# Performance work log

Measured on AMD Instinct MI355X. Metric: run time of the kernel, lower is better.

The kernel has to match this reference:

```python
import jax, jax.numpy as jnp
import numpy as np

B, T, I, H, O = 64, 512, 128, 1024, 128
FORGET_BIAS = 1.0  # TF LSTMCell default


def setup_inputs() -> dict:
    key = jax.random.key(0)
    k1, k2, k3 = jax.random.split(key, 3)
    X = jax.random.normal(k1, (B, T, I), dtype=jnp.float32)
    Wk = jax.random.normal(k2, (I + H, 4 * H), dtype=jnp.float32) * 0.02
    b = jnp.zeros((4 * H,), dtype=jnp.float32)
    Wd = jax.random.normal(k3, (H, O), dtype=jnp.float32) * 0.02
    bd = jnp.zeros((O,), dtype=jnp.float32)
    return {"X": X, "Wk": Wk, "b": b, "Wd": Wd, "bd": bd}


def _lstm(X, Wk, b):
    # TF LSTMCell with activation=relu; gate order in kernel: i, j, f, o
    batch = X.shape[0]
    h = X.shape[-1]  # not used; keep shapes explicit below
    c0 = jnp.zeros((batch, H), dtype=X.dtype)
    h0 = jnp.zeros((batch, H), dtype=X.dtype)

    def step(carry, x_t):
        c, hs = carry
        z = jnp.concatenate([x_t, hs], axis=-1) @ Wk + b  # [B, 4H]
        i, j, f, o = jnp.split(z, 4, axis=-1)
        i = jax.nn.sigmoid(i)
        f = jax.nn.sigmoid(f + FORGET_BIAS)
        o = jax.nn.sigmoid(o)
        g = jax.nn.relu(j)          # cell-input activation (custom relu)
        c_new = f * c + i * g
        h_new = o * jax.nn.relu(c_new)  # output activation (custom relu)
        return (c_new, h_new), h_new

    xs = jnp.swapaxes(X, 0, 1)  # [T, B, I]
    _, hs = jax.lax.scan(step, (c0, h0), xs)
    return jnp.swapaxes(hs, 0, 1)  # [B, T, H]


def reference(X, Wk, b, Wd, bd):
    rnn_out = _lstm(X, Wk, b)          # [B, T, H]
    outputs = rnn_out @ Wd + bd        # [B, T, O] (SL=True: dense per timestep)
    return outputs
```

## Files before the change

kernel.cpp:

```cpp
#include <hip/hip_runtime.h>
#include <math.h>

#define Bsz 64
#define Tn  512
#define In  128
#define Hn  1024
#define KT  1152
#define NBLK 128

#define GARR0 0
#define GFLG0 512

typedef __attribute__((ext_vector_type(8))) short bf16x8;
typedef __attribute__((ext_vector_type(4))) short s16x4;
typedef __attribute__((ext_vector_type(4))) float f32x4;
typedef __attribute__((ext_vector_type(4))) int   i32x4;

__device__ void llvm_amdgcn_raw_buffer_store_i16(short vdata, i32x4 srsrc, int voffset, int soffset, int cpol) __asm("llvm.amdgcn.raw.buffer.store.i16");

__device__ __forceinline__ i32x4 make_srd(const void* p, int bytes) {
  i32x4 r;
  r.x = (int)(unsigned)(unsigned long long)p;
  r.y = (int)((unsigned long long)p >> 32);
  r.z = bytes;
  r.w = 0x00020000;
  return r;
}

__device__ __forceinline__ unsigned short f2bf(float f) {
  union { float f; unsigned u; } x; x.f = f;
  unsigned r = x.u + 0x7FFFu + ((x.u >> 16) & 1u);
  return (unsigned short)(r >> 16);
}
__device__ __forceinline__ float sigmoidf_(float x) { return 1.0f / (1.0f + __expf(-x)); }

__global__ __launch_bounds__(256) void cast_x_kernel(const float* __restrict__ in,
                                                     unsigned short* __restrict__ out) {
  int i = blockIdx.x * 256 + threadIdx.x;
  f32x4 v = ((const f32x4*)in)[i];
  s16x4 o;
  o.x = (short)f2bf(v.x); o.y = (short)f2bf(v.y);
  o.z = (short)f2bf(v.z); o.w = (short)f2bf(v.w);
  ((s16x4*)out)[i] = o;
}

__global__ __launch_bounds__(256) void transpose_cast_kernel(const float* __restrict__ in,
                                                             unsigned short* __restrict__ out,
                                                             int R, int C, int ldo, int tilesR) {
  __shared__ unsigned short tile[64][73];
  int br = blockIdx.x % tilesR, bc = blockIdx.x / tilesR;
  int r0 = br << 6, c0 = bc << 6;
  for (int e = threadIdx.x; e < 4096; e += 256) {
    int r = e >> 6, c = e & 63;
    tile[r][c] = f2bf(in[(size_t)(r0 + r) * C + (c0 + c)]);
  }
  __syncthreads();
  for (int e = threadIdx.x; e < 4096; e += 256) {
    int c = e >> 6, r = e & 63;
    out[(size_t)(c0 + c) * ldo + (r0 + r)] = tile[r][c];
  }
}

__global__ __launch_bounds__(512, 1) void lstm_kernel(
    const unsigned short* __restrict__ Xb,
    const unsigned short* __restrict__ WkT,
    const float* __restrict__ bias,
    unsigned short* __restrict__ hs,
    unsigned* __restrict__ S)
{
  __shared__ float Z4[4][64][36];
  const int tid = threadIdx.x;
  const int blk = blockIdx.x;
  const int grp = blk >> 4;
  const int w   = tid >> 6;
  const int mh  = w & 1;
  const int kq  = w >> 1;
  const int l   = tid & 63, q = l >> 4, n16 = l & 15;

  const i32x4 hsrd = make_srd(hs, Tn * Bsz * Hn * 2);

  bf16x8 Bf[2][9];
#pragma unroll
  for (int nt = 0; nt < 2; ++nt) {
    int cl   = nt * 16 + n16;
    int gcol = (cl >> 3) * Hn + blk * 8 + (cl & 7);
    const unsigned short* bp = WkT + (size_t)gcol * KT + kq * 288 + q * 8;
#pragma unroll
    for (int ks = 0; ks < 9; ++ks)
      Bf[nt][ks] = *(const bf16x8*)(bp + ks * 32);
  }

  const int eb = tid >> 3, ej = tid & 7;
  const float bi  = bias[           blk * 8 + ej];
  const float bg  = bias[    Hn   + blk * 8 + ej];
  const float bfg = bias[2 * Hn   + blk * 8 + ej] + 1.0f;
  const float bo  = bias[3 * Hn   + blk * 8 + ej];
  const int   hst_off = (eb * Hn + blk * 8 + ej) * 2;
  float cst = 0.0f;

  const int b0 = mh * 32 + n16;
  const int b1 = b0 + 16;

  const unsigned needm = (kq == 0) ? 0x03u : (kq == 1) ? 0x0Eu : (kq == 2) ? 0x38u : 0xE0u;
  const bool mine = (l < 8) && ((needm >> l) & 1u);

  for (int t = 0; t < Tn; ++t) {
    f32x4 a00 = {0,0,0,0}, a01 = {0,0,0,0}, a10 = {0,0,0,0}, a11 = {0,0,0,0};

    if (t > 0) {
      bf16x8 X0[4], X1[4];
      if (kq == 0) {
#pragma unroll
        for (int ks = 0; ks < 4; ++ks) {
          X0[ks] = *(const bf16x8*)(Xb + ((size_t)b0 * Tn + t) * In + ks * 32 + q * 8);
          X1[ks] = *(const bf16x8*)(Xb + ((size_t)b1 * Tn + t) * In + ks * 32 + q * 8);
        }
      }
      for (;;) {
        unsigned f = mine ? __hip_atomic_load(&S[GFLG0 + 32 * l], __ATOMIC_RELAXED,
                                              __HIP_MEMORY_SCOPE_AGENT)
                          : 0xFFFFFFFFu;
        if (__ballot(f >= (unsigned)t) == ~0ull) break;
        __builtin_amdgcn_s_sleep(1);
      }
      const unsigned short* hrow = hs + (size_t)(t - 1) * (Bsz * Hn);
#pragma unroll
      for (int ks = 0; ks < 9; ++ks) {
        bf16x8 A0, A1;
        if (kq == 0 && ks < 4) {
          A0 = X0[ks]; A1 = X1[ks];
        } else {
          int kh = kq * 288 + ks * 32 - 128 + q * 8;
          A0 = *(const bf16x8*)(hrow + (size_t)b0 * Hn + kh);
          A1 = *(const bf16x8*)(hrow + (size_t)b1 * Hn + kh);
        }
        a00 = __builtin_amdgcn_mfma_f32_16x16x32_bf16(A0, Bf[0][ks], a00, 0, 0, 0);
        a01 = __builtin_amdgcn_mfma_f32_16x16x32_bf16(A0, Bf[1][ks], a01, 0, 0, 0);
        a10 = __builtin_amdgcn_mfma_f32_16x16x32_bf16(A1, Bf[0][ks], a10, 0, 0, 0);
        a11 = __builtin_amdgcn_mfma_f32_16x16x32_bf16(A1, Bf[1][ks], a11, 0, 0, 0);
      }
    } else if (kq == 0) {
#pragma unroll
      for (int ks = 0; ks < 4; ++ks) {
        bf16x8 A0 = *(const bf16x8*)(Xb + ((size_t)b0 * Tn) * In + ks * 32 + q * 8);
        bf16x8 A1 = *(const bf16x8*)(Xb + ((size_t)b1 * Tn) * In + ks * 32 + q * 8);
        a00 = __builtin_amdgcn_mfma_f32_16x16x32_bf16(A0, Bf[0][ks], a00, 0, 0, 0);
        a01 = __builtin_amdgcn_mfma_f32_16x16x32_bf16(A0, Bf[1][ks], a01, 0, 0, 0);
        a10 = __builtin_amdgcn_mfma_f32_16x16x32_bf16(A1, Bf[0][ks], a10, 0, 0, 0);
        a11 = __builtin_amdgcn_mfma_f32_16x16x32_bf16(A1, Bf[1][ks], a11, 0, 0, 0);
      }
    }

#pragma unroll
    for (int r = 0; r < 4; ++r) {
      int row = mh * 32 + q * 4 + r;
      Z4[kq][row     ][     n16] = a00[r];
      Z4[kq][row     ][16 + n16] = a01[r];
      Z4[kq][row + 16][     n16] = a10[r];
      Z4[kq][row + 16][16 + n16] = a11[r];
    }
    __syncthreads();

    float zi = bi, zg = bg, zf = bfg, zo = bo;
#pragma unroll
    for (int k2 = 0; k2 < 4; ++k2) {
      zi += Z4[k2][eb][     ej];
      zg += Z4[k2][eb][ 8 + ej];
      zf += Z4[k2][eb][16 + ej];
      zo += Z4[k2][eb][24 + ej];
    }
    float ig = sigmoidf_(zi);
    float g  = fmaxf(zg, 0.0f);
    float ff = sigmoidf_(zf);
    float oo = sigmoidf_(zo);
    cst = ff * cst + ig * g;
    float hn = oo * fmaxf(cst, 0.0f);
    llvm_amdgcn_raw_buffer_store_i16((short)f2bf(hn), hsrd,
                                     t * (Bsz * Hn * 2) + hst_off, 0, 17);

    __syncthreads();
    if (t < Tn - 1 && tid == 0) {
      const unsigned tgt = (unsigned)t + 1u;
      unsigned old = __hip_atomic_fetch_add(&S[GARR0 + 32 * grp], 1u,
                                            __ATOMIC_RELAXED, __HIP_MEMORY_SCOPE_AGENT);
      if (old == 16u * tgt - 1u)
        __hip_atomic_store(&S[GFLG0 + 32 * grp], tgt,
                           __ATOMIC_RELAXED, __HIP_MEMORY_SCOPE_AGENT);
    }
  }
}

__global__ __launch_bounds__(256) void dense_kernel(
    const unsigned short* __restrict__ hs,
    const unsigned short* __restrict__ WdT,
    const float* __restrict__ bd,
    float* __restrict__ out)
{
  const int tid = threadIdx.x;
  const int w = tid >> 6, l = tid & 63, q = l >> 4, n16 = l & 15;
  const int R0 = blockIdx.x * 64 + w * 16;
  f32x4 acc[8];
#pragma unroll
  for (int i = 0; i < 8; ++i) acc[i] = (f32x4){0, 0, 0, 0};
  const unsigned short* arow = hs + (size_t)(R0 + n16) * Hn + q * 8;
#pragma unroll 4
  for (int ks = 0; ks < 32; ++ks) {
    bf16x8 A = *(const bf16x8*)(arow + ks * 32);
#pragma unroll
    for (int nt = 0; nt < 8; ++nt) {
      bf16x8 Bf = *(const bf16x8*)(WdT + (size_t)(nt * 16 + n16) * Hn + ks * 32 + q * 8);
      acc[nt] = __builtin_amdgcn_mfma_f32_16x16x32_bf16(A, Bf, acc[nt], 0, 0, 0);
    }
  }
#pragma unroll
  for (int nt = 0; nt < 8; ++nt) {
    int col = nt * 16 + n16;
    float bdv = bd[col];
#pragma unroll
    for (int r = 0; r < 4; ++r) {
      int R = R0 + q * 4 + r;
      int b = R & 63, t = R >> 6;
      out[((size_t)b * Tn + t) * 128 + col] = acc[nt][r] + bdv;
    }
  }
}

extern "C" void kernel_launch(void* const* d_in, const int* in_sizes, int n_in,
                              void* d_out, int out_size, void* d_ws, size_t ws_size,
                              hipStream_t stream) {
  const float* X    = (const float*)d_in[0];
  const float* Wk   = (const float*)d_in[1];
  const float* bias = (const float*)d_in[2];
  const float* Wd   = (const float*)d_in[3];
  const float* bd   = (const float*)d_in[4];
  float* out = (float*)d_out;

  char* ws = (char*)d_ws;
  unsigned short* Xb  = (unsigned short*)(ws);
  unsigned short* WkT = (unsigned short*)(ws + 8388608);
  unsigned short* WdT = (unsigned short*)(ws + 17825792);
  unsigned short* hs  = (unsigned short*)(ws + 18087936);
  unsigned*       syn = (unsigned*)      (ws + 85196800);

  hipMemsetAsync(syn, 0, 4096, stream);
  cast_x_kernel<<<4096, 256, 0, stream>>>(X, Xb);
  transpose_cast_kernel<<<1152, 256, 0, stream>>>(Wk, WkT, 1152, 4096, 1152, 18);
  transpose_cast_kernel<<<32, 256, 0, stream>>>(Wd, WdT, 1024, 128, 1024, 16);
  lstm_kernel<<<NBLK, 512, 0, stream>>>(Xb, WkT, bias, hs, syn);
  dense_kernel<<<512, 256, 0, stream>>>(hs, WdT, bd, out);
}
```

Before: 3.027 ms.

## Replace atomic counter barrier with per-block flags and vectorized h stores

Drops the per-group atomic fetch_add arrival counter and flag. Each block now writes its own step flag with a plain store, issued by lane 0 after a vmcnt(0) wait. Consumers poll the flags of the blocks they depend on with 16-byte buffer loads and take the min in registers. The h output is first staged in LDS, then written with one 16-byte store per batch row instead of scattered 2-byte stores. This removes the atomic serialization and a hop from the inter-block handoff, but now relies on the wait inside one wave to order the other waves' stores ahead of the flag, which is a memory-ordering risk.

After: 4.061 ms. 34.2% more time.

```diff
diff --git a/kernel.cpp b/kernel.cpp
--- a/kernel.cpp
+++ b/kernel.cpp
@@ -8,15 +8,15 @@
 #define KT  1152
 #define NBLK 128
 
-#define GARR0 0
-#define GFLG0 512
 
 typedef __attribute__((ext_vector_type(8))) short bf16x8;
 typedef __attribute__((ext_vector_type(4))) short s16x4;
 typedef __attribute__((ext_vector_type(4))) float f32x4;
 typedef __attribute__((ext_vector_type(4))) int   i32x4;
 
-__device__ void llvm_amdgcn_raw_buffer_store_i16(short vdata, i32x4 srsrc, int voffset, int soffset, int cpol) __asm("llvm.amdgcn.raw.buffer.store.i16");
+__device__ void llvm_amdgcn_raw_buffer_store_v4i32(i32x4 vdata, i32x4 srsrc, int voffset, int soffset, int cpol) __asm("llvm.amdgcn.raw.buffer.store.v4i32");
+__device__ void llvm_amdgcn_raw_buffer_store_i32(int vdata, i32x4 srsrc, int voffset, int soffset, int cpol) __asm("llvm.amdgcn.raw.buffer.store.i32");
+__device__ i32x4 llvm_amdgcn_raw_buffer_load_v4i32(i32x4 srsrc, int voffset, int soffset, int cpol) __asm("llvm.amdgcn.raw.buffer.load.v4i32");
 
 __device__ __forceinline__ i32x4 make_srd(const void* p, int bytes) {
   i32x4 r;
@@ -69,15 +69,16 @@
     unsigned* __restrict__ S)
 {
   __shared__ float Z4[4][64][36];
+  __shared__ __align__(16) unsigned short Hl[64][8];
   const int tid = threadIdx.x;
   const int blk = blockIdx.x;
-  const int grp = blk >> 4;
   const int w   = tid >> 6;
   const int mh  = w & 1;
   const int kq  = w >> 1;
   const int l   = tid & 63, q = l >> 4, n16 = l & 15;
 
   const i32x4 hsrd = make_srd(hs, Tn * Bsz * Hn * 2);
+  const i32x4 fsrd = make_srd(S, 2048);
 
   bf16x8 Bf[2][9];
 #pragma unroll
@@ -95,14 +96,13 @@
   const float bg  = bias[    Hn   + blk * 8 + ej];
   const float bfg = bias[2 * Hn   + blk * 8 + ej] + 1.0f;
   const float bo  = bias[3 * Hn   + blk * 8 + ej];
-  const int   hst_off = (eb * Hn + blk * 8 + ej) * 2;
   float cst = 0.0f;
 
   const int b0 = mh * 32 + n16;
   const int b1 = b0 + 16;
 
-  const unsigned needm = (kq == 0) ? 0x03u : (kq == 1) ? 0x0Eu : (kq == 2) ? 0x38u : 0xE0u;
-  const bool mine = (l < 8) && ((needm >> l) & 1u);
+  const int gbase = (kq == 0) ? 0 : (5 + (kq - 1) * 9);
+  const int ng    = kq ? 9 : 5;
 
   for (int t = 0; t < Tn; ++t) {
     f32x4 a00 = {0,0,0,0}, a01 = {0,0,0,0}, a10 = {0,0,0,0}, a11 = {0,0,0,0};
@@ -117,10 +117,17 @@
         }
       }
       for (;;) {
-        unsigned f = mine ? __hip_atomic_load(&S[GFLG0 + 32 * l], __ATOMIC_RELAXED,
-                                              __HIP_MEMORY_SCOPE_AGENT)
-                          : 0xFFFFFFFFu;
-        if (__ballot(f >= (unsigned)t) == ~0ull) break;
+        asm volatile("" ::: "memory");
+        unsigned m = 0xFFFFFFFFu;
+        if (l < ng) {
+          i32x4 v = llvm_amdgcn_raw_buffer_load_v4i32(fsrd, (gbase + l) << 4, 0, 17);
+          unsigned ma = (unsigned)v.x, mb = (unsigned)v.y;
+          unsigned mc = (unsigned)v.z, md = (unsigned)v.w;
+          ma = ma < mb ? ma : mb;
+          mc = mc < md ? mc : md;
+          m  = ma < mc ? ma : mc;
+        }
+        if (__ballot(m >= (unsigned)t) == ~0ull) break;
         __builtin_amdgcn_s_sleep(1);
       }
       const unsigned short* hrow = hs + (size_t)(t - 1) * (Bsz * Hn);
@@ -175,17 +182,16 @@
     float oo = sigmoidf_(zo);
     cst = ff * cst + ig * g;
     float hn = oo * fmaxf(cst, 0.0f);
-    llvm_amdgcn_raw_buffer_store_i16((short)f2bf(hn), hsrd,
-                                     t * (Bsz * Hn * 2) + hst_off, 0, 17);
-
+    Hl[eb][ej] = f2bf(hn);
     __syncthreads();
-    if (t < Tn - 1 && tid == 0) {
-      const unsigned tgt = (unsigned)t + 1u;
-      unsigned old = __hip_atomic_fetch_add(&S[GARR0 + 32 * grp], 1u,
-                                            __ATOMIC_RELAXED, __HIP_MEMORY_SCOPE_AGENT);
-      if (old == 16u * tgt - 1u)
-        __hip_atomic_store(&S[GFLG0 + 32 * grp], tgt,
-                           __ATOMIC_RELAXED, __HIP_MEMORY_SCOPE_AGENT);
+
+    if (tid < 64) {
+      i32x4 hv = *(const i32x4*)(&Hl[tid][0]);
+      llvm_amdgcn_raw_buffer_store_v4i32(hv, hsrd,
+          t * (Bsz * Hn * 2) + (tid * Hn + blk * 8) * 2, 0, 17);
+      asm volatile("s_waitcnt vmcnt(0)" ::: "memory");
+      if (tid == 0 && t < Tn - 1)
+        llvm_amdgcn_raw_buffer_store_i32(t + 1, fsrd, blk << 2, 0, 17);
     }
   }
 }
```

## Rebalance K split across waves and poll arrival counters directly instead of flags

Applied to the files above, without the earlier changes.

Re-splits the K dimension so each of the four K-quarter waves takes 32 input columns plus 256 hidden columns. The old split gave wave 0 all 128 input columns, so its hidden slices straddled group boundaries and needed flags from up to three groups. Each wave now waits on exactly two group counters. The separate flag word, which the last arriving block had to set, is gone: waiters poll the arrival counter against 16*t, removing the second store from the critical path between timesteps. It also adds unconditional per-step X loads for every wave, and spinning now happens on a counter that is also being atomically incremented.

After: 3.602 ms. 19.0% more time.

```diff
diff --git a/kernel.cpp b/kernel.cpp
--- a/kernel.cpp
+++ b/kernel.cpp
@@ -9,7 +9,6 @@
 #define NBLK 128
 
 #define GARR0 0
-#define GFLG0 512
 
 typedef __attribute__((ext_vector_type(8))) short bf16x8;
 typedef __attribute__((ext_vector_type(4))) short s16x4;
@@ -84,10 +83,11 @@
   for (int nt = 0; nt < 2; ++nt) {
     int cl   = nt * 16 + n16;
     int gcol = (cl >> 3) * Hn + blk * 8 + (cl & 7);
-    const unsigned short* bp = WkT + (size_t)gcol * KT + kq * 288 + q * 8;
-#pragma unroll
-    for (int ks = 0; ks < 9; ++ks)
-      Bf[nt][ks] = *(const bf16x8*)(bp + ks * 32);
+    const unsigned short* bp = WkT + (size_t)gcol * KT;
+    Bf[nt][0] = *(const bf16x8*)(bp + kq * 32 + q * 8);
+#pragma unroll
+    for (int ks = 1; ks < 9; ++ks)
+      Bf[nt][ks] = *(const bf16x8*)(bp + 128 + kq * 256 + (ks - 1) * 32 + q * 8);
   }
 
   const int eb = tid >> 3, ej = tid & 7;
@@ -101,54 +101,41 @@
   const int b0 = mh * 32 + n16;
   const int b1 = b0 + 16;
 
-  const unsigned needm = (kq == 0) ? 0x03u : (kq == 1) ? 0x0Eu : (kq == 2) ? 0x38u : 0xE0u;
-  const bool mine = (l < 8) && ((needm >> l) & 1u);
-
   for (int t = 0; t < Tn; ++t) {
     f32x4 a00 = {0,0,0,0}, a01 = {0,0,0,0}, a10 = {0,0,0,0}, a11 = {0,0,0,0};
 
+    bf16x8 X0 = *(const bf16x8*)(Xb + ((size_t)b0 * Tn + t) * In + kq * 32 + q * 8);
+    bf16x8 X1 = *(const bf16x8*)(Xb + ((size_t)b1 * Tn + t) * In + kq * 32 + q * 8);
+
     if (t > 0) {
-      bf16x8 X0[4], X1[4];
-      if (kq == 0) {
-#pragma unroll
-        for (int ks = 0; ks < 4; ++ks) {
-          X0[ks] = *(const bf16x8*)(Xb + ((size_t)b0 * Tn + t) * In + ks * 32 + q * 8);
-          X1[ks] = *(const bf16x8*)(Xb + ((size_t)b1 * Tn + t) * In + ks * 32 + q * 8);
-        }
-      }
+      const unsigned tgt = 16u * (unsigned)t;
       for (;;) {
-        unsigned f = mine ? __hip_atomic_load(&S[GFLG0 + 32 * l], __ATOMIC_RELAXED,
-                                              __HIP_MEMORY_SCOPE_AGENT)
-                          : 0xFFFFFFFFu;
-        if (__ballot(f >= (unsigned)t) == ~0ull) break;
+        unsigned f = (l < 2) ? __hip_atomic_load(&S[GARR0 + 32 * (2 * kq + l)],
+                                                 __ATOMIC_RELAXED, __HIP_MEMORY_SCOPE_AGENT)
+                             : 0xFFFFFFFFu;
+        if (__ballot(f >= tgt) == ~0ull) break;
         __builtin_amdgcn_s_sleep(1);
       }
       const unsigned short* hrow = hs + (size_t)(t - 1) * (Bsz * Hn);
-#pragma unroll
-      for (int ks = 0; ks < 9; ++ks) {
-        bf16x8 A0, A1;
-        if (kq == 0 && ks < 4) {
-          A0 = X0[ks]; A1 = X1[ks];
-        } else {
-          int kh = kq * 288 + ks * 32 - 128 + q * 8;
-          A0 = *(const bf16x8*)(hrow + (size_t)b0 * Hn + kh);
-          A1 = *(const bf16x8*)(hrow + (size_t)b1 * Hn + kh);
-        }
+      a00 = __builtin_amdgcn_mfma_f32_16x16x32_bf16(X0, Bf[0][0], a00, 0, 0, 0);
+      a01 = __builtin_amdgcn_mfma_f32_16x16x32_bf16(X0, Bf[1][0], a01, 0, 0, 0);
+      a10 = __builtin_amdgcn_mfma_f32_16x16x32_bf16(X1, Bf[0][0], a10, 0, 0, 0);
+      a11 = __builtin_amdgcn_mfma_f32_16x16x32_bf16(X1, Bf[1][0], a11, 0, 0, 0);
+#pragma unroll
+      for (int ks = 1; ks < 9; ++ks) {
+        int kh = kq * 256 + (ks - 1) * 32 + q * 8;
+        bf16x8 A0 = *(const bf16x8*)(hrow + (size_t)b0 * Hn + kh);
+        bf16x8 A1 = *(const bf16x8*)(hrow + (size_t)b1 * Hn + kh);
         a00 = __builtin_amdgcn_mfma_f32_16x16x32_bf16(A0, Bf[0][ks], a00, 0, 0, 0);
         a01 = __builtin_amdgcn_mfma_f32_16x16x32_bf16(A0, Bf[1][ks], a01, 0, 0, 0);
         a10 = __builtin_amdgcn_mfma_f32_16x16x32_bf16(A1, Bf[0][ks], a10, 0, 0, 0);
         a11 = __builtin_amdgcn_mfma_f32_16x16x32_bf16(A1, Bf[1][ks], a11, 0, 0, 0);
       }
-    } else if (kq == 0) {
-#pragma unroll
-      for (int ks = 0; ks < 4; ++ks) {
-        bf16x8 A0 = *(const bf16x8*)(Xb + ((size_t)b0 * Tn) * In + ks * 32 + q * 8);
-        bf16x8 A1 = *(const bf16x8*)(Xb + ((size_t)b1 * Tn) * In + ks * 32 + q * 8);
-        a00 = __builtin_amdgcn_mfma_f32_16x16x32_bf16(A0, Bf[0][ks], a00, 0, 0, 0);
-        a01 = __builtin_amdgcn_mfma_f32_16x16x32_bf16(A0, Bf[1][ks], a01, 0, 0, 0);
-        a10 = __builtin_amdgcn_mfma_f32_16x16x32_bf16(A1, Bf[0][ks], a10, 0, 0, 0);
-        a11 = __builtin_amdgcn_mfma_f32_16x16x32_bf16(A1, Bf[1][ks], a11, 0, 0, 0);
-      }
+    } else {
+      a00 = __builtin_amdgcn_mfma_f32_16x16x32_bf16(X0, Bf[0][0], a00, 0, 0, 0);
+      a01 = __builtin_amdgcn_mfma_f32_16x16x32_bf16(X0, Bf[1][0], a01, 0, 0, 0);
+      a10 = __builtin_amdgcn_mfma_f32_16x16x32_bf16(X1, Bf[0][0], a10, 0, 0, 0);
+      a11 = __builtin_amdgcn_mfma_f32_16x16x32_bf16(X1, Bf[1][0], a11, 0, 0, 0);
     }
 
 #pragma unroll
@@ -180,12 +167,8 @@
 
     __syncthreads();
     if (t < Tn - 1 && tid == 0) {
-      const unsigned tgt = (unsigned)t + 1u;
-      unsigned old = __hip_atomic_fetch_add(&S[GARR0 + 32 * grp], 1u,
-                                            __ATOMIC_RELAXED, __HIP_MEMORY_SCOPE_AGENT);
-      if (old == 16u * tgt - 1u)
-        __hip_atomic_store(&S[GFLG0 + 32 * grp], tgt,
-                           __ATOMIC_RELAXED, __HIP_MEMORY_SCOPE_AGENT);
+      (void)__hip_atomic_fetch_add(&S[GARR0 + 32 * grp], 1u,
+                                   __ATOMIC_RELAXED, __HIP_MEMORY_SCOPE_AGENT);
     }
   }
 }
```

## Split LSTM block into independent batch halves with wave-pair LDS handoff

Applied to the files above, without the earlier changes.

Reduces the LSTM block from 8 waves to 4. Each half-batch (32 rows) becomes an independent pair of waves with its own global counters and flags, so the two batch halves advance without a block-wide barrier. Within a pair, the wave holding the X part and the first 448 h columns hands its partial sums to the other wave through LDS and a workgroup-scope flag, replacing __syncthreads. Each wave also waits only on the producer groups whose h columns it actually reads. The cost is fewer waves per block, a doubled per-wave K length (more serial MFMA work and more weight registers), and spin-waits on LDS flags.

Measured after the change: 4.113 ms. 35.9% more time.

```diff
diff --git a/kernel.cpp b/kernel.cpp
--- a/kernel.cpp
+++ b/kernel.cpp
@@ -8,8 +8,8 @@
 #define KT  1152
 #define NBLK 128
 
-#define GARR0 0
-#define GFLG0 512
+#define CNT(s,g) (32 * ((s) * 8 + (g)))
+#define FLG(s,g) (512 + 32 * ((s) * 8 + (g)))
 
 typedef __attribute__((ext_vector_type(8))) short bf16x8;
 typedef __attribute__((ext_vector_type(4))) short s16x4;
@@ -61,131 +61,154 @@
   }
 }
 
-__global__ __launch_bounds__(512, 1) void lstm_kernel(
+__global__ __launch_bounds__(256, 1) void lstm_kernel(
     const unsigned short* __restrict__ Xb,
     const unsigned short* __restrict__ WkT,
     const float* __restrict__ bias,
     unsigned short* __restrict__ hs,
     unsigned* __restrict__ S)
 {
-  __shared__ float Z4[4][64][36];
+  __shared__ float Zx[2][64][16];
+  __shared__ float Zw[2][32][33];
+  __shared__ unsigned FlL[2][32];
+
   const int tid = threadIdx.x;
   const int blk = blockIdx.x;
   const int grp = blk >> 4;
   const int w   = tid >> 6;
-  const int mh  = w & 1;
-  const int kq  = w >> 1;
+  const int s   = w >> 1;
+  const int kh  = w & 1;
   const int l   = tid & 63, q = l >> 4, n16 = l & 15;
 
   const i32x4 hsrd = make_srd(hs, Tn * Bsz * Hn * 2);
 
-  bf16x8 Bf[2][9];
+  if (tid < 64) { FlL[0][tid >> 5] = 0; FlL[1][tid >> 5] = 0; }
+  __syncthreads();
+
+  const int k0 = kh ? 0 : 576;
+  bf16x8 Bf[2][18];
 #pragma unroll
   for (int nt = 0; nt < 2; ++nt) {
     int cl   = nt * 16 + n16;
     int gcol = (cl >> 3) * Hn + blk * 8 + (cl & 7);
-    const unsigned short* bp = WkT + (size_t)gcol * KT + kq * 288 + q * 8;
-#pragma unroll
-    for (int ks = 0; ks < 9; ++ks)
+    const unsigned short* bp = WkT + (size_t)gcol * KT + k0 + q * 8;
+#pragma unroll
+    for (int ks = 0; ks < 18; ++ks)
       Bf[nt][ks] = *(const bf16x8*)(bp + ks * 32);
   }
 
-  const int eb = tid >> 3, ej = tid & 7;
+  const int ej = l & 7, er = l >> 3;
   const float bi  = bias[           blk * 8 + ej];
   const float bg  = bias[    Hn   + blk * 8 + ej];
   const float bfg = bias[2 * Hn   + blk * 8 + ej] + 1.0f;
   const float bo  = bias[3 * Hn   + blk * 8 + ej];
-  const int   hst_off = (eb * Hn + blk * 8 + ej) * 2;
-  float cst = 0.0f;
-
-  const int b0 = mh * 32 + n16;
+  float cst[4] = {0.0f, 0.0f, 0.0f, 0.0f};
+
+  const int b0 = s * 32 + n16;
   const int b1 = b0 + 16;
-
-  const unsigned needm = (kq == 0) ? 0x03u : (kq == 1) ? 0x0Eu : (kq == 2) ? 0x38u : 0xE0u;
-  const bool mine = (l < 8) && ((needm >> l) & 1u);
 
   for (int t = 0; t < Tn; ++t) {
     f32x4 a00 = {0,0,0,0}, a01 = {0,0,0,0}, a10 = {0,0,0,0}, a11 = {0,0,0,0};
 
-    if (t > 0) {
-      bf16x8 X0[4], X1[4];
-      if (kq == 0) {
-#pragma unroll
-        for (int ks = 0; ks < 4; ++ks) {
-          X0[ks] = *(const bf16x8*)(Xb + ((size_t)b0 * Tn + t) * In + ks * 32 + q * 8);
-          X1[ks] = *(const bf16x8*)(Xb + ((size_t)b1 * Tn + t) * In + ks * 32 + q * 8);
-        }
-      }
-      for (;;) {
-        unsigned f = mine ? __hip_atomic_load(&S[GFLG0 + 32 * l], __ATOMIC_RELAXED,
-                                              __HIP_MEMORY_SCOPE_AGENT)
-                          : 0xFFFFFFFFu;
-        if (__ballot(f >= (unsigned)t) == ~0ull) break;
-        __builtin_amdgcn_s_sleep(1);
-      }
-      const unsigned short* hrow = hs + (size_t)(t - 1) * (Bsz * Hn);
-#pragma unroll
-      for (int ks = 0; ks < 9; ++ks) {
-        bf16x8 A0, A1;
-        if (kq == 0 && ks < 4) {
-          A0 = X0[ks]; A1 = X1[ks];
-        } else {
-          int kh = kq * 288 + ks * 32 - 128 + q * 8;
-          A0 = *(const bf16x8*)(hrow + (size_t)b0 * Hn + kh);
-          A1 = *(const bf16x8*)(hrow + (size_t)b1 * Hn + kh);
-        }
+    if (kh == 1) {
+#pragma unroll
+      for (int ks = 0; ks < 4; ++ks) {
+        bf16x8 A0 = *(const bf16x8*)(Xb + ((size_t)b0 * Tn + t) * In + ks * 32 + q * 8);
+        bf16x8 A1 = *(const bf16x8*)(Xb + ((size_t)b1 * Tn + t) * In + ks * 32 + q * 8);
         a00 = __builtin_amdgcn_mfma_f32_16x16x32_bf16(A0, Bf[0][ks], a00, 0, 0, 0);
         a01 = __builtin_amdgcn_mfma_f32_16x16x32_bf16(A0, Bf[1][ks], a01, 0, 0, 0);
         a10 = __builtin_amdgcn_mfma_f32_16x16x32_bf16(A1, Bf[0][ks], a10, 0, 0, 0);
         a11 = __builtin_amdgcn_mfma_f32_16x16x32_bf16(A1, Bf[1][ks], a11, 0, 0, 0);
       }
-    } else if (kq == 0) {
-#pragma unroll
-      for (int ks = 0; ks < 4; ++ks) {
-        bf16x8 A0 = *(const bf16x8*)(Xb + ((size_t)b0 * Tn) * In + ks * 32 + q * 8);
-        bf16x8 A1 = *(const bf16x8*)(Xb + ((size_t)b1 * Tn) * In + ks * 32 + q * 8);
-        a00 = __builtin_amdgcn_mfma_f32_16x16x32_bf16(A0, Bf[0][ks], a00, 0, 0, 0);
-        a01 = __builtin_amdgcn_mfma_f32_16x16x32_bf16(A0, Bf[1][ks], a01, 0, 0, 0);
-        a10 = __builtin_amdgcn_mfma_f32_16x16x32_bf16(A1, Bf[0][ks], a10, 0, 0, 0);
-        a11 = __builtin_amdgcn_mfma_f32_16x16x32_bf16(A1, Bf[1][ks], a11, 0, 0, 0);
-      }
-    }
-
-#pragma unroll
-    for (int r = 0; r < 4; ++r) {
-      int row = mh * 32 + q * 4 + r;
-      Z4[kq][row     ][     n16] = a00[r];
-      Z4[kq][row     ][16 + n16] = a01[r];
-      Z4[kq][row + 16][     n16] = a10[r];
-      Z4[kq][row + 16][16 + n16] = a11[r];
-    }
-    __syncthreads();
-
-    float zi = bi, zg = bg, zf = bfg, zo = bo;
-#pragma unroll
-    for (int k2 = 0; k2 < 4; ++k2) {
-      zi += Z4[k2][eb][     ej];
-      zg += Z4[k2][eb][ 8 + ej];
-      zf += Z4[k2][eb][16 + ej];
-      zo += Z4[k2][eb][24 + ej];
-    }
-    float ig = sigmoidf_(zi);
-    float g  = fmaxf(zg, 0.0f);
-    float ff = sigmoidf_(zf);
-    float oo = sigmoidf_(zo);
-    cst = ff * cst + ig * g;
-    float hn = oo * fmaxf(cst, 0.0f);
-    llvm_amdgcn_raw_buffer_store_i16((short)f2bf(hn), hsrd,
-                                     t * (Bsz * Hn * 2) + hst_off, 0, 17);
-
-    __syncthreads();
-    if (t < Tn - 1 && tid == 0) {
-      const unsigned tgt = (unsigned)t + 1u;
-      unsigned old = __hip_atomic_fetch_add(&S[GARR0 + 32 * grp], 1u,
-                                            __ATOMIC_RELAXED, __HIP_MEMORY_SCOPE_AGENT);
-      if (old == 16u * tgt - 1u)
-        __hip_atomic_store(&S[GFLG0 + 32 * grp], tgt,
-                           __ATOMIC_RELAXED, __HIP_MEMORY_SCOPE_AGENT);
+      if (t > 0) {
+        for (;;) {
+          unsigned f = (l < 4) ? __hip_atomic_load(&S[FLG(s, l)], __ATOMIC_RELAXED,
+                                                   __HIP_MEMORY_SCOPE_AGENT)
+                               : 0xFFFFFFFFu;
+          if (__ballot(f >= (unsigned)t) == ~0ull) break;
+          __builtin_amdgcn_s_sleep(1);
+        }
+        const unsigned short* hrow = hs + (size_t)(t - 1) * (Bsz * Hn);
+#pragma unroll
+        for (int ks = 4; ks < 18; ++ks) {
+          int kcol = (ks - 4) * 32 + q * 8;
+          bf16x8 A0 = *(const bf16x8*)(hrow + (size_t)b0 * Hn + kcol);
+          bf16x8 A1 = *(const bf16x8*)(hrow + (size_t)b1 * Hn + kcol);
+          a00 = __builtin_amdgcn_mfma_f32_16x16x32_bf16(A0, Bf[0][ks], a00, 0, 0, 0);
+          a01 = __builtin_amdgcn_mfma_f32_16x16x32_bf16(A0, Bf[1][ks], a01, 0, 0, 0);
+          a10 = __builtin_amdgcn_mfma_f32_16x16x32_bf16(A1, Bf[0][ks], a10, 0, 0, 0);
+          a11 = __builtin_amdgcn_mfma_f32_16x16x32_bf16(A1, Bf[1][ks], a11, 0, 0, 0);
+        }
+      }
+      *(f32x4*)(&Zx[s][l][ 0]) = a00;
+      *(f32x4*)(&Zx[s][l][ 4]) = a01;
+      *(f32x4*)(&Zx[s][l][ 8]) = a10;
+      *(f32x4*)(&Zx[s][l][12]) = a11;
+      asm volatile("s_waitcnt lgkmcnt(0)" ::: "memory");
+      __hip_atomic_store(&FlL[s][0], (unsigned)(t + 1), __ATOMIC_RELAXED,
+                         __HIP_MEMORY_SCOPE_WORKGROUP);
+    } else {
+      if (t > 0) {
+        for (;;) {
+          unsigned f = (l < 5) ? __hip_atomic_load(&S[FLG(s, 3 + l)], __ATOMIC_RELAXED,
+                                                   __HIP_MEMORY_SCOPE_AGENT)
+                               : 0xFFFFFFFFu;
+          if (__ballot(f >= (unsigned)t) == ~0ull) break;
+          __builtin_amdgcn_s_sleep(1);
+        }
+        const unsigned short* hrow = hs + (size_t)(t - 1) * (Bsz * Hn);
+#pragma unroll
+        for (int ks = 0; ks < 18; ++ks) {
+          int kcol = 448 + ks * 32 + q * 8;
+          bf16x8 A0 = *(const bf16x8*)(hrow + (size_t)b0 * Hn + kcol);
+          bf16x8 A1 = *(const bf16x8*)(hrow + (size_t)b1 * Hn + kcol);
+          a00 = __builtin_amdgcn_mfma_f32_16x16x32_bf16(A0, Bf[0][ks], a00, 0, 0, 0);
+          a01 = __builtin_amdgcn_mfma_f32_16x16x32_bf16(A0, Bf[1][ks], a01, 0, 0, 0);
+          a10 = __builtin_amdgcn_mfma_f32_16x16x32_bf16(A1, Bf[0][ks], a10, 0, 0, 0);
+          a11 = __builtin_amdgcn_mfma_f32_16x16x32_bf16(A1, Bf[1][ks], a11, 0, 0, 0);
+        }
+      }
+      while (__hip_atomic_load(&FlL[s][0], __ATOMIC_RELAXED,
+                               __HIP_MEMORY_SCOPE_WORKGROUP) < (unsigned)(t + 1)) { }
+      asm volatile("" ::: "memory");
+      a00 += *(const f32x4*)(&Zx[s][l][ 0]);
+      a01 += *(const f32x4*)(&Zx[s][l][ 4]);
+      a10 += *(const f32x4*)(&Zx[s][l][ 8]);
+      a11 += *(const f32x4*)(&Zx[s][l][12]);
+
+#pragma unroll
+      for (int r = 0; r < 4; ++r) {
+        Zw[s][     q * 4 + r][     n16] = a00[r];
+        Zw[s][     q * 4 + r][16 + n16] = a01[r];
+        Zw[s][16 + q * 4 + r][     n16] = a10[r];
+        Zw[s][16 + q * 4 + r][16 + n16] = a11[r];
+      }
+      asm volatile("s_waitcnt lgkmcnt(0)" ::: "memory");
+
+#pragma unroll
+      for (int c = 0; c < 4; ++c) {
+        int row = er + 8 * c;
+        float zi = Zw[s][row][     ej] + bi;
+        float zg = Zw[s][row][ 8 + ej] + bg;
+        float zf = Zw[s][row][16 + ej] + bfg;
+        float zo = Zw[s][row][24 + ej] + bo;
+        float ig = sigmoidf_(zi);
+        float g  = fmaxf(zg, 0.0f);
+        float ff = sigmoidf_(zf);
+        float oo = sigmoidf_(zo);
+        cst[c] = ff * cst[c] + ig * g;
+        float hn = oo * fmaxf(cst[c], 0.0f);
+        llvm_amdgcn_raw_buffer_store_i16((short)f2bf(hn), hsrd,
+            t * (Bsz * Hn * 2) + ((s * 32 + row) * Hn + blk * 8 + ej) * 2, 0, 17);
+      }
+      asm volatile("s_waitcnt vmcnt(0)" ::: "memory");
+      if (t < Tn - 1 && l == 0) {
+        unsigned old = __hip_atomic_fetch_add(&S[CNT(s, grp)], 1u,
+                                              __ATOMIC_RELAXED, __HIP_MEMORY_SCOPE_AGENT);
+        if (old == 16u * (unsigned)(t + 1) - 1u)
+          __hip_atomic_store(&S[FLG(s, grp)], (unsigned)(t + 1),
+                             __ATOMIC_RELAXED, __HIP_MEMORY_SCOPE_AGENT);
+      }
     }
   }
 }
@@ -246,6 +269,6 @@
   cast_x_kernel<<<4096, 256, 0, stream>>>(X, Xb);
   transpose_cast_kernel<<<1152, 256, 0, stream>>>(Wk, WkT, 1152, 4096, 1152, 18);
   transpose_cast_kernel<<<32, 256, 0, stream>>>(Wd, WdT, 1024, 128, 1024, 16);
-  lstm_kernel<<<NBLK, 512, 0, stream>>>(Xb, WkT, bias, hs, syn);
+  lstm_kernel<<<NBLK, 256, 0, stream>>>(Xb, WkT, bias, hs, syn);
   dense_kernel<<<512, 256, 0, stream>>>(hs, WdT, bd, out);
 }
```
